# Performance work log

Measured on AMD Instinct MI355X. Metric: run time of the kernel, lower is better.

Reference implementation:

```python
import jax, jax.numpy as jnp
import numpy as np

EPS = 1e-8

def setup_inputs() -> dict:
    key = jax.random.key(0)
    k1, k2, k3, k4 = jax.random.split(key, 4)
    B, S, D = 64, 512, 512
    emb1 = jax.random.normal(k1, (B, S, D), dtype=jnp.float32)
    emb2 = jax.random.normal(k2, (B, S, D), dtype=jnp.float32)
    # contiguous prefix attention masks (first n tokens valid), as assumed by the original
    len1 = jax.random.randint(k3, (B,), S // 4, S + 1)
    len2 = jax.random.randint(k4, (B,), S // 4, S + 1)
    pos = jnp.arange(S)
    mask1 = (pos[None, :] < len1[:, None]).astype(jnp.int32)
    mask2 = (pos[None, :] < len2[:, None]).astype(jnp.int32)
    return {"article_1_emb": emb1, "article_2_emb": emb2,
            "article_1_att_mask": mask1, "article_2_att_mask": mask2}


def reference(article_1_emb, article_2_emb, article_1_att_mask, article_2_att_mask):
    # L2-normalize token embeddings (cosine similarity = dot of normalized vectors)
    def l2n(x):
        n = jnp.sqrt(jnp.sum(x * x, axis=-1, keepdims=True))
        return x / jnp.maximum(n, EPS)

    e1 = l2n(article_1_emb)   # [B, S1, D]
    e2 = l2n(article_2_emb)   # [B, S2, D]
    sim = jnp.einsum('bid,bjd->bij', e1, e2)  # [B, S1, S2] pairwise cosine sims

    m1 = article_1_att_mask.astype(jnp.bool_)  # [B, S1]
    m2 = article_2_att_mask.astype(jnp.bool_)  # [B, S2]
    NEG = jnp.float32(-1e9)

    # max over valid j for each valid i, and max over valid i for each valid j
    row_max = jnp.max(jnp.where(m2[:, None, :], sim, NEG), axis=2)  # [B, S1]
    col_max = jnp.max(jnp.where(m1[:, :, None], sim, NEG), axis=1)  # [B, S2]
    row_sum = jnp.sum(jnp.where(m1, row_max, 0.0), axis=1)          # [B]
    col_sum = jnp.sum(jnp.where(m2, col_max, 0.0), axis=1)          # [B]

    n1 = jnp.sum(article_1_att_mask, axis=1).astype(jnp.float32)
    n2 = jnp.sum(article_2_att_mask, axis=1).astype(jnp.float32)
    return (row_sum + col_sum) / (n1 + n2)
```

## Files before the change

### kernel.cpp

```cpp
#include <hip/hip_runtime.h>
#include <hip/hip_bf16.h>


typedef __attribute__((ext_vector_type(8))) short bf16x8;
typedef __attribute__((ext_vector_type(4))) float f32x4;

#define NEGBIG (-1e9f)
#define CAST_LDS(p) ((__attribute__((address_space(3))) void*)(p))
#define CAST_G(p)   ((const __attribute__((address_space(1))) void*)(p))

__device__ __forceinline__ unsigned bfbits(float f) {
    union { float f; unsigned u; } c; c.f = f;
    return (c.u + 0x7fffu + ((c.u >> 16) & 1u)) >> 16;
}
__device__ __forceinline__ unsigned packbf(float lo, float hi) {
    return (bfbits(hi) << 16) | bfbits(lo);
}

__global__ __launch_bounds__(256)
void prep_kernel(const float* __restrict__ e1, const float* __restrict__ e2,
                 ushort* __restrict__ n1, ushort* __restrict__ n2,
                 float* __restrict__ inv1, float* __restrict__ inv2)
{
    const int lane = threadIdx.x & 63;
    const int w    = threadIdx.x >> 6;
    const int row  = blockIdx.x * 4 + w;
    const bool is1 = row < 32768;
    const int  r   = is1 ? row : row - 32768;
    const float* src = (is1 ? e1 : e2) + (size_t)r * 512;
    ushort*      dst = (is1 ? n1 : n2) + (size_t)r * 512;

    const float4* s4 = reinterpret_cast<const float4*>(src);
    float4 a = s4[lane * 2];
    float4 c = s4[lane * 2 + 1];

    uint4 p;
    p.x = packbf(a.x, a.y);
    p.y = packbf(a.z, a.w);
    p.z = packbf(c.x, c.y);
    p.w = packbf(c.z, c.w);
    reinterpret_cast<uint4*>(dst)[lane] = p;

    float ss = a.x*a.x + a.y*a.y + a.z*a.z + a.w*a.w
             + c.x*c.x + c.y*c.y + c.z*c.z + c.w*c.w;
    #pragma unroll
    for (int m = 32; m; m >>= 1) ss += __shfl_xor(ss, m);
    if (lane == 0) {
        float iv = 1.0f / fmaxf(sqrtf(ss), 1e-8f);
        (is1 ? inv1 : inv2)[r] = iv;
    }
}

__global__ __launch_bounds__(256, 2)
void sim_kernel(const ushort* __restrict__ n1, const ushort* __restrict__ n2,
                const int* __restrict__ m1g, const int* __restrict__ m2g,
                const float* __restrict__ inv1, const float* __restrict__ inv2,
                float* __restrict__ rowmax_p,
                float* __restrict__ colmax_p)
{
    const int rt  = blockIdx.x;
    const int ct  = blockIdx.y;
    const int b   = blockIdx.z;
    const int tid = threadIdx.x;
    const int lane = tid & 63;
    const int w    = tid >> 6;
    const int wm   = w >> 1;
    const int wn   = w & 1;
    const int q    = lane >> 4;
    const int ln   = lane & 15;

    __shared__ __align__(16) ushort sA[128 * 32];
    __shared__ __align__(16) ushort sB[128 * 32];
    __shared__ float spr[2][128];
    __shared__ float spc[2][128];
    __shared__ int   sm1[128];
    __shared__ int   sm2[512];
    __shared__ float sinv1[128];
    __shared__ float sinv2[512];

    if (tid < 128) {
        sm1[tid]   = m1g[b * 512 + rt * 128 + tid];
        sinv1[tid] = inv1[b * 512 + rt * 128 + tid];
    }
    sm2[tid]         = m2g[b * 512 + tid];
    sm2[tid + 256]   = m2g[b * 512 + tid + 256];
    sinv2[tid]       = inv2[b * 512 + tid];
    sinv2[tid + 256] = inv2[b * 512 + tid + 256];

    const int gc = (lane & 3) ^ ((lane >> 2) & 3) ^ ((lane >> 4) & 3);
    const int r0 = w * 16 + (lane >> 2);
    const ushort* gA0 = n1 + (size_t)(b * 512 + rt * 128 + r0) * 512 + gc * 8;
    const ushort* gA1 = gA0 + 64 * 512;
    ushort* lA0 = sA + w * 512;
    ushort* lA1 = sA + 2048 + w * 512;
    ushort* lB0 = sB + w * 512;
    ushort* lB1 = sB + 2048 + w * 512;

    const int sln = (ln & 3) ^ ((ln >> 2) & 3);
    const ushort* aptr[4];
    const ushort* bptr[4];
    #pragma unroll
    for (int mt = 0; mt < 4; ++mt)
        aptr[mt] = &sA[(wm * 64 + mt * 16 + ln) * 32 + ((q ^ sln) << 3)];
    #pragma unroll
    for (int nt = 0; nt < 4; ++nt)
        bptr[nt] = &sB[(wn * 64 + nt * 16 + ln) * 32 + ((q ^ sln) << 3)];

    float runrow = NEGBIG;

    for (int nc = 0; nc < 2; ++nc) {
        const int nb = ct * 256 + nc * 128;
        const ushort* gB0 = n2 + (size_t)(b * 512 + nb + r0) * 512 + gc * 8;
        const ushort* gB1 = gB0 + 64 * 512;

        f32x4 acc[4][4];
        #pragma unroll
        for (int i = 0; i < 4; ++i)
            #pragma unroll
            for (int j = 0; j < 4; ++j)
                acc[i][j] = (f32x4){0.f, 0.f, 0.f, 0.f};

        for (int k0 = 0; k0 < 512; k0 += 32) {
            __syncthreads();
            __builtin_amdgcn_global_load_lds(CAST_G(gA0 + k0), CAST_LDS(lA0), 16, 0, 0);
            __builtin_amdgcn_global_load_lds(CAST_G(gA1 + k0), CAST_LDS(lA1), 16, 0, 0);
            __builtin_amdgcn_global_load_lds(CAST_G(gB0 + k0), CAST_LDS(lB0), 16, 0, 0);
            __builtin_amdgcn_global_load_lds(CAST_G(gB1 + k0), CAST_LDS(lB1), 16, 0, 0);
            __syncthreads();

            bf16x8 af[4], bfr[4];
            #pragma unroll
            for (int mt = 0; mt < 4; ++mt)
                af[mt] = *reinterpret_cast<const bf16x8*>(aptr[mt]);
            #pragma unroll
            for (int nt = 0; nt < 4; ++nt)
                bfr[nt] = *reinterpret_cast<const bf16x8*>(bptr[nt]);
            #pragma unroll
            for (int mt = 0; mt < 4; ++mt)
                #pragma unroll
                for (int nt = 0; nt < 4; ++nt)
                    acc[mt][nt] = __builtin_amdgcn_mfma_f32_16x16x32_bf16(
                        af[mt], bfr[nt], acc[mt][nt], 0, 0, 0);
        }

        float invj[4];
        f32x4 invi[4];
        #pragma unroll
        for (int nt = 0; nt < 4; ++nt)
            invj[nt] = sinv2[nb + wn * 64 + nt * 16 + ln];
        #pragma unroll
        for (int mt = 0; mt < 4; ++mt)
            #pragma unroll
            for (int rg = 0; rg < 4; ++rg)
                invi[mt][rg] = sinv1[wm * 64 + mt * 16 + q * 4 + rg];
        #pragma unroll
        for (int mt = 0; mt < 4; ++mt)
            #pragma unroll
            for (int nt = 0; nt < 4; ++nt)
                acc[mt][nt] = acc[mt][nt] * (invi[mt] * invj[nt]);

        #pragma unroll
        for (int mt = 0; mt < 4; ++mt) {
            #pragma unroll
            for (int rg = 0; rg < 4; ++rg) {
                float rm = NEGBIG;
                #pragma unroll
                for (int nt = 0; nt < 4; ++nt) {
                    int j = nb + wn * 64 + nt * 16 + ln;
                    float s = sm2[j] ? acc[mt][nt][rg] : NEGBIG;
                    rm = fmaxf(rm, s);
                }
                rm = fmaxf(rm, __shfl_xor(rm, 1));
                rm = fmaxf(rm, __shfl_xor(rm, 2));
                rm = fmaxf(rm, __shfl_xor(rm, 4));
                rm = fmaxf(rm, __shfl_xor(rm, 8));
                if (ln == 0) spr[wn][wm * 64 + mt * 16 + q * 4 + rg] = rm;
            }
        }
        #pragma unroll
        for (int nt = 0; nt < 4; ++nt) {
            float cm = NEGBIG;
            #pragma unroll
            for (int mt = 0; mt < 4; ++mt)
                #pragma unroll
                for (int rg = 0; rg < 4; ++rg) {
                    int il = wm * 64 + mt * 16 + q * 4 + rg;
                    float s = sm1[il] ? acc[mt][nt][rg] : NEGBIG;
                    cm = fmaxf(cm, s);
                }
            cm = fmaxf(cm, __shfl_xor(cm, 16));
            cm = fmaxf(cm, __shfl_xor(cm, 32));
            if (lane < 16) spc[wm][wn * 64 + nt * 16 + ln] = cm;
        }
        __syncthreads();
        if (tid < 128) {
            runrow = fmaxf(runrow, fmaxf(spr[0][tid], spr[1][tid]));
            colmax_p[((size_t)b * 4 + rt) * 512 + nb + tid] =
                fmaxf(spc[0][tid], spc[1][tid]);
        }
        __syncthreads();
    }
    if (tid < 128)
        rowmax_p[((size_t)b * 2 + ct) * 512 + rt * 128 + tid] = runrow;
}

__global__ __launch_bounds__(256)
void final_kernel(const int* __restrict__ m1g, const int* __restrict__ m2g,
                  const float* __restrict__ rowmax_p, const float* __restrict__ colmax_p,
                  float* __restrict__ out)
{
    const int b = blockIdx.x;
    const int tid = threadIdx.x;
    const int lane = tid & 63;
    const int w = tid >> 6;

    float sum = 0.f;
    float nn  = 0.f;
    for (int j = tid; j < 512; j += 256) {
        int mm1 = m1g[b * 512 + j];
        int mm2 = m2g[b * 512 + j];
        nn += (float)(mm1 + mm2);
        float rm = fmaxf(rowmax_p[(size_t)b * 1024 + j],
                         rowmax_p[(size_t)b * 1024 + 512 + j]);
        if (mm1) sum += rm;
        const float* cp = colmax_p + (size_t)b * 2048 + j;
        float cm = fmaxf(fmaxf(cp[0], cp[512]), fmaxf(cp[1024], cp[1536]));
        if (mm2) sum += cm;
    }
    #pragma unroll
    for (int m = 32; m; m >>= 1) {
        sum += __shfl_xor(sum, m);
        nn  += __shfl_xor(nn, m);
    }
    __shared__ float ssum[4], snn[4];
    if (lane == 0) { ssum[w] = sum; snn[w] = nn; }
    __syncthreads();
    if (tid == 0) {
        float S = ssum[0] + ssum[1] + ssum[2] + ssum[3];
        float N = snn[0] + snn[1] + snn[2] + snn[3];
        out[b] = S / N;
    }
}

__global__ __launch_bounds__(256)
void norm_kernel(const float* __restrict__ e1, const float* __restrict__ e2,
                 float* __restrict__ inv1, float* __restrict__ inv2)
{
    const int lane = threadIdx.x & 63;
    const int w    = threadIdx.x >> 6;
    const int row  = blockIdx.x * 4 + w;
    const float* src = (row < 32768) ? (e1 + (size_t)row * 512)
                                     : (e2 + (size_t)(row - 32768) * 512);
    const float4* s4 = reinterpret_cast<const float4*>(src);
    float4 a = s4[lane];
    float4 c = s4[lane + 64];
    float ss = a.x*a.x + a.y*a.y + a.z*a.z + a.w*a.w
             + c.x*c.x + c.y*c.y + c.z*c.z + c.w*c.w;
    #pragma unroll
    for (int m = 32; m; m >>= 1) ss += __shfl_xor(ss, m);
    if (lane == 0) {
        float iv = 1.0f / fmaxf(sqrtf(ss), 1e-8f);
        if (row < 32768) inv1[row] = iv; else inv2[row - 32768] = iv;
    }
}

__global__ __launch_bounds__(256, 2)
void sim_kernel_f32(const float* __restrict__ e1, const float* __restrict__ e2,
                    const int* __restrict__ m1g, const int* __restrict__ m2g,
                    const float* __restrict__ inv1, const float* __restrict__ inv2,
                    float* __restrict__ rowmax_p, float* __restrict__ colmax_p)
{
    const int rt  = blockIdx.x;
    const int ct  = blockIdx.y;
    const int b   = blockIdx.z;
    const int tid = threadIdx.x;
    const int lane = tid & 63;
    const int w    = tid >> 6;
    const int wm   = w >> 1;
    const int wn   = w & 1;
    const int q    = lane >> 4;
    const int ln   = lane & 15;

    __shared__ __align__(16) short sA[128 * 40];
    __shared__ __align__(16) short sB[128 * 40];
    __shared__ float spr[2][128];
    __shared__ float spc[2][128];
    __shared__ int   sm1[128];
    __shared__ int   sm2[512];

    if (tid < 128) sm1[tid] = m1g[b * 512 + rt * 128 + tid];
    sm2[tid]       = m2g[b * 512 + tid];
    sm2[tid + 256] = m2g[b * 512 + tid + 256];

    const int rA = tid >> 1;
    const int h  = tid & 1;
    const size_t baseA = ((size_t)(b * 512 + rt * 128 + rA)) * 512 + h * 16;
    const float iA = inv1[b * 512 + rt * 128 + rA];

    float runrow = NEGBIG;

    for (int nc = 0; nc < 2; ++nc) {
        const int nb = ct * 256 + nc * 128;
        const size_t baseB = ((size_t)(b * 512 + nb + rA)) * 512 + h * 16;
        const float iB = inv2[b * 512 + nb + rA];

        f32x4 acc[4][4];
        #pragma unroll
        for (int i = 0; i < 4; ++i)
            #pragma unroll
            for (int j = 0; j < 4; ++j)
                acc[i][j] = (f32x4){0.f, 0.f, 0.f, 0.f};

        for (int k0 = 0; k0 < 512; k0 += 32) {
            __syncthreads();
            {
                const float4* s4 = reinterpret_cast<const float4*>(e1 + baseA + k0);
                float4 v0 = s4[0], v1 = s4[1], v2 = s4[2], v3 = s4[3];
                uint4 p;
                p.x = packbf(v0.x * iA, v0.y * iA);
                p.y = packbf(v0.z * iA, v0.w * iA);
                p.z = packbf(v1.x * iA, v1.y * iA);
                p.w = packbf(v1.z * iA, v1.w * iA);
                *reinterpret_cast<uint4*>(&sA[rA * 40 + h * 16]) = p;
                p.x = packbf(v2.x * iA, v2.y * iA);
                p.y = packbf(v2.z * iA, v2.w * iA);
                p.z = packbf(v3.x * iA, v3.y * iA);
                p.w = packbf(v3.z * iA, v3.w * iA);
                *reinterpret_cast<uint4*>(&sA[rA * 40 + h * 16 + 8]) = p;
            }
            {
                const float4* s4 = reinterpret_cast<const float4*>(e2 + baseB + k0);
                float4 v0 = s4[0], v1 = s4[1], v2 = s4[2], v3 = s4[3];
                uint4 p;
                p.x = packbf(v0.x * iB, v0.y * iB);
                p.y = packbf(v0.z * iB, v0.w * iB);
                p.z = packbf(v1.x * iB, v1.y * iB);
                p.w = packbf(v1.z * iB, v1.w * iB);
                *reinterpret_cast<uint4*>(&sB[rA * 40 + h * 16]) = p;
                p.x = packbf(v2.x * iB, v2.y * iB);
                p.y = packbf(v2.z * iB, v2.w * iB);
                p.z = packbf(v3.x * iB, v3.y * iB);
                p.w = packbf(v3.z * iB, v3.w * iB);
                *reinterpret_cast<uint4*>(&sB[rA * 40 + h * 16 + 8]) = p;
            }
            __syncthreads();
            bf16x8 af[4], bfr[4];
            #pragma unroll
            for (int mt = 0; mt < 4; ++mt)
                af[mt] = *reinterpret_cast<const bf16x8*>(&sA[(wm * 64 + mt * 16 + ln) * 40 + q * 8]);
            #pragma unroll
            for (int nt = 0; nt < 4; ++nt)
                bfr[nt] = *reinterpret_cast<const bf16x8*>(&sB[(wn * 64 + nt * 16 + ln) * 40 + q * 8]);
            #pragma unroll
            for (int mt = 0; mt < 4; ++mt)
                #pragma unroll
                for (int nt = 0; nt < 4; ++nt)
                    acc[mt][nt] = __builtin_amdgcn_mfma_f32_16x16x32_bf16(
                        af[mt], bfr[nt], acc[mt][nt], 0, 0, 0);
        }

        #pragma unroll
        for (int mt = 0; mt < 4; ++mt) {
            #pragma unroll
            for (int rg = 0; rg < 4; ++rg) {
                float rm = NEGBIG;
                #pragma unroll
                for (int nt = 0; nt < 4; ++nt) {
                    int j = nb + wn * 64 + nt * 16 + ln;
                    float s = sm2[j] ? acc[mt][nt][rg] : NEGBIG;
                    rm = fmaxf(rm, s);
                }
                rm = fmaxf(rm, __shfl_xor(rm, 1));
                rm = fmaxf(rm, __shfl_xor(rm, 2));
                rm = fmaxf(rm, __shfl_xor(rm, 4));
                rm = fmaxf(rm, __shfl_xor(rm, 8));
                if (ln == 0) spr[wn][wm * 64 + mt * 16 + q * 4 + rg] = rm;
            }
        }
        #pragma unroll
        for (int nt = 0; nt < 4; ++nt) {
            float cm = NEGBIG;
            #pragma unroll
            for (int mt = 0; mt < 4; ++mt)
                #pragma unroll
                for (int rg = 0; rg < 4; ++rg) {
                    int il = wm * 64 + mt * 16 + q * 4 + rg;
                    float s = sm1[il] ? acc[mt][nt][rg] : NEGBIG;
                    cm = fmaxf(cm, s);
                }
            cm = fmaxf(cm, __shfl_xor(cm, 16));
            cm = fmaxf(cm, __shfl_xor(cm, 32));
            if (lane < 16) spc[wm][wn * 64 + nt * 16 + ln] = cm;
        }
        __syncthreads();
        if (tid < 128) {
            runrow = fmaxf(runrow, fmaxf(spr[0][tid], spr[1][tid]));
            colmax_p[((size_t)b * 4 + rt) * 512 + nb + tid] =
                fmaxf(spc[0][tid], spc[1][tid]);
        }
        __syncthreads();
    }
    if (tid < 128)
        rowmax_p[((size_t)b * 2 + ct) * 512 + rt * 128 + tid] = runrow;
}

extern "C" void kernel_launch(void* const* d_in, const int* in_sizes, int n_in,
                              void* d_out, int out_size, void* d_ws, size_t ws_size,
                              hipStream_t stream) {
    const float* e1 = (const float*)d_in[0];
    const float* e2 = (const float*)d_in[1];
    const int*   m1 = (const int*)d_in[2];
    const int*   m2 = (const int*)d_in[3];
    float* out = (float*)d_out;

    const size_t NELEM = (size_t)64 * 512 * 512;
    const size_t need  = 2 * NELEM * sizeof(ushort)
                       + (32768 + 32768 + 65536 + 131072) * sizeof(float);

    if (ws_size >= need) {
        ushort* n1 = (ushort*)d_ws;
        ushort* n2 = n1 + NELEM;
        float* tail     = (float*)(n2 + NELEM);
        float* inv1     = tail;
        float* inv2     = tail + 32768;
        float* rowmax_p = tail + 65536;
        float* colmax_p = tail + 131072;
        prep_kernel<<<16384, 256, 0, stream>>>(e1, e2, n1, n2, inv1, inv2);
        sim_kernel<<<dim3(4, 2, 64), 256, 0, stream>>>(n1, n2, m1, m2, inv1, inv2,
                                                       rowmax_p, colmax_p);
        final_kernel<<<64, 256, 0, stream>>>(m1, m2, rowmax_p, colmax_p, out);
    } else {
        float* ws = (float*)d_ws;
        float* inv1     = ws;
        float* inv2     = ws + 32768;
        float* rowmax_p = ws + 65536;
        float* colmax_p = ws + 131072;
        norm_kernel<<<16384, 256, 0, stream>>>(e1, e2, inv1, inv2);
        sim_kernel_f32<<<dim3(4, 2, 64), 256, 0, stream>>>(e1, e2, m1, m2, inv1, inv2,
                                                           rowmax_p, colmax_p);
        final_kernel<<<64, 256, 0, stream>>>(m1, m2, rowmax_p, colmax_p, out);
    }
}
```

Measured before the change: 195.7 us.

## Double-buffer LDS in sim kernel, split column tiles, process two rows per prep wave

```diff
diff --git a/kernel.cpp b/kernel.cpp
--- a/kernel.cpp
+++ b/kernel.cpp
@@ -16,42 +16,62 @@
 __device__ __forceinline__ unsigned packbf(float lo, float hi) {
     return (bfbits(hi) << 16) | bfbits(lo);
 }
-
-__global__ __launch_bounds__(256)
+__device__ __forceinline__ unsigned packbf2_hw(float lo, float hi) {
+    __hip_bfloat162 h = __float22bfloat162_rn(float2{lo, hi});
+    union { __hip_bfloat162 h; unsigned u; } c; c.h = h;
+    return c.u;
+}
+
+__global__ __launch_bounds__(256, 4)
 void prep_kernel(const float* __restrict__ e1, const float* __restrict__ e2,
                  ushort* __restrict__ n1, ushort* __restrict__ n2,
                  float* __restrict__ inv1, float* __restrict__ inv2)
 {
     const int lane = threadIdx.x & 63;
     const int w    = threadIdx.x >> 6;
-    const int row  = blockIdx.x * 4 + w;
-    const bool is1 = row < 32768;
-    const int  r   = is1 ? row : row - 32768;
+    const int gw   = blockIdx.x * 4 + w;
+    const int row0 = gw * 2;
+    const bool is1 = row0 < 32768;
+    const int  r   = is1 ? row0 : row0 - 32768;
     const float* src = (is1 ? e1 : e2) + (size_t)r * 512;
     ushort*      dst = (is1 ? n1 : n2) + (size_t)r * 512;
-
-    const float4* s4 = reinterpret_cast<const float4*>(src);
-    float4 a = s4[lane * 2];
-    float4 c = s4[lane * 2 + 1];
-
-    uint4 p;
-    p.x = packbf(a.x, a.y);
-    p.y = packbf(a.z, a.w);
-    p.z = packbf(c.x, c.y);
-    p.w = packbf(c.z, c.w);
-    reinterpret_cast<uint4*>(dst)[lane] = p;
-
-    float ss = a.x*a.x + a.y*a.y + a.z*a.z + a.w*a.w
-             + c.x*c.x + c.y*c.y + c.z*c.z + c.w*c.w;
-    #pragma unroll
-    for (int m = 32; m; m >>= 1) ss += __shfl_xor(ss, m);
+    float*      invp = (is1 ? inv1 : inv2) + r;
+
+    float4 v[2][2];
+    #pragma unroll
+    for (int rr = 0; rr < 2; ++rr) {
+        const float4* s4 = reinterpret_cast<const float4*>(src + rr * 512);
+        v[rr][0] = s4[lane * 2];
+        v[rr][1] = s4[lane * 2 + 1];
+    }
+    #pragma unroll
+    for (int rr = 0; rr < 2; ++rr) {
+        uint4 p;
+        p.x = packbf2_hw(v[rr][0].x, v[rr][0].y);
+        p.y = packbf2_hw(v[rr][0].z, v[rr][0].w);
+        p.z = packbf2_hw(v[rr][1].x, v[rr][1].y);
+        p.w = packbf2_hw(v[rr][1].z, v[rr][1].w);
+        reinterpret_cast<uint4*>(dst + rr * 512)[lane] = p;
+    }
+    float ss[2];
+    #pragma unroll
+    for (int rr = 0; rr < 2; ++rr) {
+        float4 a = v[rr][0], c = v[rr][1];
+        ss[rr] = a.x*a.x + a.y*a.y + a.z*a.z + a.w*a.w
+               + c.x*c.x + c.y*c.y + c.z*c.z + c.w*c.w;
+    }
+    #pragma unroll
+    for (int m = 32; m; m >>= 1) {
+        ss[0] += __shfl_xor(ss[0], m);
+        ss[1] += __shfl_xor(ss[1], m);
+    }
     if (lane == 0) {
-        float iv = 1.0f / fmaxf(sqrtf(ss), 1e-8f);
-        (is1 ? inv1 : inv2)[r] = iv;
-    }
-}
-
-__global__ __launch_bounds__(256, 2)
+        invp[0] = 1.0f / fmaxf(sqrtf(ss[0]), 1e-8f);
+        invp[1] = 1.0f / fmaxf(sqrtf(ss[1]), 1e-8f);
+    }
+}
+
+__global__ __launch_bounds__(256, 4)
 void sim_kernel(const ushort* __restrict__ n1, const ushort* __restrict__ n2,
                 const int* __restrict__ m1g, const int* __restrict__ m2g,
                 const float* __restrict__ inv1, const float* __restrict__ inv2,
@@ -68,140 +88,133 @@
     const int wn   = w & 1;
     const int q    = lane >> 4;
     const int ln   = lane & 15;
-
-    __shared__ __align__(16) ushort sA[128 * 32];
-    __shared__ __align__(16) ushort sB[128 * 32];
+    const int nb   = ct * 128;
+
+    __shared__ __align__(16) ushort sA[2][128 * 32];
+    __shared__ __align__(16) ushort sB[2][128 * 32];
     __shared__ float spr[2][128];
     __shared__ float spc[2][128];
-    __shared__ int   sm1[128];
-    __shared__ int   sm2[512];
-    __shared__ float sinv1[128];
-    __shared__ float sinv2[512];
+    __shared__ int   sm1[128], sm2[128];
+    __shared__ float sinv1[128], sinv2[128];
 
     if (tid < 128) {
         sm1[tid]   = m1g[b * 512 + rt * 128 + tid];
         sinv1[tid] = inv1[b * 512 + rt * 128 + tid];
-    }
-    sm2[tid]         = m2g[b * 512 + tid];
-    sm2[tid + 256]   = m2g[b * 512 + tid + 256];
-    sinv2[tid]       = inv2[b * 512 + tid];
-    sinv2[tid + 256] = inv2[b * 512 + tid + 256];
+    } else {
+        int t = tid - 128;
+        sm2[t]   = m2g[b * 512 + nb + t];
+        sinv2[t] = inv2[b * 512 + nb + t];
+    }
 
     const int gc = (lane & 3) ^ ((lane >> 2) & 3) ^ ((lane >> 4) & 3);
     const int r0 = w * 16 + (lane >> 2);
     const ushort* gA0 = n1 + (size_t)(b * 512 + rt * 128 + r0) * 512 + gc * 8;
     const ushort* gA1 = gA0 + 64 * 512;
-    ushort* lA0 = sA + w * 512;
-    ushort* lA1 = sA + 2048 + w * 512;
-    ushort* lB0 = sB + w * 512;
-    ushort* lB1 = sB + 2048 + w * 512;
+    const ushort* gB0 = n2 + (size_t)(b * 512 + nb + r0) * 512 + gc * 8;
+    const ushort* gB1 = gB0 + 64 * 512;
 
     const int sln = (ln & 3) ^ ((ln >> 2) & 3);
-    const ushort* aptr[4];
-    const ushort* bptr[4];
+    int aoff[4], boff[4];
     #pragma unroll
     for (int mt = 0; mt < 4; ++mt)
-        aptr[mt] = &sA[(wm * 64 + mt * 16 + ln) * 32 + ((q ^ sln) << 3)];
+        aoff[mt] = (wm * 64 + mt * 16 + ln) * 32 + ((q ^ sln) << 3);
     #pragma unroll
     for (int nt = 0; nt < 4; ++nt)
-        bptr[nt] = &sB[(wn * 64 + nt * 16 + ln) * 32 + ((q ^ sln) << 3)];
-
-    float runrow = NEGBIG;
-
-    for (int nc = 0; nc < 2; ++nc) {
-        const int nb = ct * 256 + nc * 128;
-        const ushort* gB0 = n2 + (size_t)(b * 512 + nb + r0) * 512 + gc * 8;
-        const ushort* gB1 = gB0 + 64 * 512;
-
-        f32x4 acc[4][4];
-        #pragma unroll
-        for (int i = 0; i < 4; ++i)
-            #pragma unroll
-            for (int j = 0; j < 4; ++j)
-                acc[i][j] = (f32x4){0.f, 0.f, 0.f, 0.f};
-
-        for (int k0 = 0; k0 < 512; k0 += 32) {
-            __syncthreads();
-            __builtin_amdgcn_global_load_lds(CAST_G(gA0 + k0), CAST_LDS(lA0), 16, 0, 0);
-            __builtin_amdgcn_global_load_lds(CAST_G(gA1 + k0), CAST_LDS(lA1), 16, 0, 0);
-            __builtin_amdgcn_global_load_lds(CAST_G(gB0 + k0), CAST_LDS(lB0), 16, 0, 0);
-            __builtin_amdgcn_global_load_lds(CAST_G(gB1 + k0), CAST_LDS(lB1), 16, 0, 0);
-            __syncthreads();
-
-            bf16x8 af[4], bfr[4];
-            #pragma unroll
-            for (int mt = 0; mt < 4; ++mt)
-                af[mt] = *reinterpret_cast<const bf16x8*>(aptr[mt]);
+        boff[nt] = (wn * 64 + nt * 16 + ln) * 32 + ((q ^ sln) << 3);
+
+    f32x4 acc[4][4];
+    #pragma unroll
+    for (int i = 0; i < 4; ++i)
+        #pragma unroll
+        for (int j = 0; j < 4; ++j)
+            acc[i][j] = (f32x4){0.f, 0.f, 0.f, 0.f};
+
+    __builtin_amdgcn_global_load_lds(CAST_G(gA0), CAST_LDS(&sA[0][w * 512]), 16, 0, 0);
+    __builtin_amdgcn_global_load_lds(CAST_G(gA1), CAST_LDS(&sA[0][2048 + w * 512]), 16, 0, 0);
+    __builtin_amdgcn_global_load_lds(CAST_G(gB0), CAST_LDS(&sB[0][w * 512]), 16, 0, 0);
+    __builtin_amdgcn_global_load_lds(CAST_G(gB1), CAST_LDS(&sB[0][2048 + w * 512]), 16, 0, 0);
+    __syncthreads();
+
+    #pragma unroll 2
+    for (int k = 0; k < 16; ++k) {
+        const int p = k & 1;
+        if (k < 15) {
+            const int k1 = (k + 1) * 32;
+            __builtin_amdgcn_global_load_lds(CAST_G(gA0 + k1), CAST_LDS(&sA[p ^ 1][w * 512]), 16, 0, 0);
+            __builtin_amdgcn_global_load_lds(CAST_G(gA1 + k1), CAST_LDS(&sA[p ^ 1][2048 + w * 512]), 16, 0, 0);
+            __builtin_amdgcn_global_load_lds(CAST_G(gB0 + k1), CAST_LDS(&sB[p ^ 1][w * 512]), 16, 0, 0);
+            __builtin_amdgcn_global_load_lds(CAST_G(gB1 + k1), CAST_LDS(&sB[p ^ 1][2048 + w * 512]), 16, 0, 0);
+        }
+        bf16x8 af[4], bfr[4];
+        #pragma unroll
+        for (int mt = 0; mt < 4; ++mt)
+            af[mt] = *reinterpret_cast<const bf16x8*>(&sA[p][aoff[mt]]);
+        #pragma unroll
+        for (int nt = 0; nt < 4; ++nt)
+            bfr[nt] = *reinterpret_cast<const bf16x8*>(&sB[p][boff[nt]]);
+        #pragma unroll
+        for (int mt = 0; mt < 4; ++mt)
             #pragma unroll
             for (int nt = 0; nt < 4; ++nt)
-                bfr[nt] = *reinterpret_cast<const bf16x8*>(bptr[nt]);
-            #pragma unroll
-            for (int mt = 0; mt < 4; ++mt)
-                #pragma unroll
-                for (int nt = 0; nt < 4; ++nt)
-                    acc[mt][nt] = __builtin_amdgcn_mfma_f32_16x16x32_bf16(
-                        af[mt], bfr[nt], acc[mt][nt], 0, 0, 0);
-        }
-
-        float invj[4];
-        f32x4 invi[4];
+                acc[mt][nt] = __builtin_amdgcn_mfma_f32_16x16x32_bf16(
+                    af[mt], bfr[nt], acc[mt][nt], 0, 0, 0);
+        __syncthreads();
+    }
+
+    float invj[4];
+    f32x4 invi[4];
+    #pragma unroll
+    for (int nt = 0; nt < 4; ++nt)
+        invj[nt] = sinv2[wn * 64 + nt * 16 + ln];
+    #pragma unroll
+    for (int mt = 0; mt < 4; ++mt)
+        #pragma unroll
+        for (int rg = 0; rg < 4; ++rg)
+            invi[mt][rg] = sinv1[wm * 64 + mt * 16 + q * 4 + rg];
+    #pragma unroll
+    for (int mt = 0; mt < 4; ++mt)
         #pragma unroll
         for (int nt = 0; nt < 4; ++nt)
-            invj[nt] = sinv2[nb + wn * 64 + nt * 16 + ln];
+            acc[mt][nt] = acc[mt][nt] * (invi[mt] * invj[nt]);
+
+    #pragma unroll
+    for (int mt = 0; mt < 4; ++mt) {
+        #pragma unroll
+        for (int rg = 0; rg < 4; ++rg) {
+            float rm = NEGBIG;
+            #pragma unroll
+            for (int nt = 0; nt < 4; ++nt) {
+                float s = sm2[wn * 64 + nt * 16 + ln] ? acc[mt][nt][rg] : NEGBIG;
+                rm = fmaxf(rm, s);
+            }
+            rm = fmaxf(rm, __shfl_xor(rm, 1));
+            rm = fmaxf(rm, __shfl_xor(rm, 2));
+            rm = fmaxf(rm, __shfl_xor(rm, 4));
+            rm = fmaxf(rm, __shfl_xor(rm, 8));
+            if (ln == 0) spr[wn][wm * 64 + mt * 16 + q * 4 + rg] = rm;
+        }
+    }
+    #pragma unroll
+    for (int nt = 0; nt < 4; ++nt) {
+        float cm = NEGBIG;
         #pragma unroll
         for (int mt = 0; mt < 4; ++mt)
             #pragma unroll
-            for (int rg = 0; rg < 4; ++rg)
-                invi[mt][rg] = sinv1[wm * 64 + mt * 16 + q * 4 + rg];
-        #pragma unroll
-        for (int mt = 0; mt < 4; ++mt)
-            #pragma unroll
-            for (int nt = 0; nt < 4; ++nt)
-                acc[mt][nt] = acc[mt][nt] * (invi[mt] * invj[nt]);
-
-        #pragma unroll
-        for (int mt = 0; mt < 4; ++mt) {
-            #pragma unroll
             for (int rg = 0; rg < 4; ++rg) {
-                float rm = NEGBIG;
-                #pragma unroll
-                for (int nt = 0; nt < 4; ++nt) {
-                    int j = nb + wn * 64 + nt * 16 + ln;
-                    float s = sm2[j] ? acc[mt][nt][rg] : NEGBIG;
-                    rm = fmaxf(rm, s);
-                }
-                rm = fmaxf(rm, __shfl_xor(rm, 1));
-                rm = fmaxf(rm, __shfl_xor(rm, 2));
-                rm = fmaxf(rm, __shfl_xor(rm, 4));
-                rm = fmaxf(rm, __shfl_xor(rm, 8));
-                if (ln == 0) spr[wn][wm * 64 + mt * 16 + q * 4 + rg] = rm;
+                float s = sm1[wm * 64 + mt * 16 + q * 4 + rg] ? acc[mt][nt][rg] : NEGBIG;
+                cm = fmaxf(cm, s);
             }
-        }
-        #pragma unroll
-        for (int nt = 0; nt < 4; ++nt) {
-            float cm = NEGBIG;
-            #pragma unroll
-            for (int mt = 0; mt < 4; ++mt)
-                #pragma unroll
-                for (int rg = 0; rg < 4; ++rg) {
-                    int il = wm * 64 + mt * 16 + q * 4 + rg;
-                    float s = sm1[il] ? acc[mt][nt][rg] : NEGBIG;
-                    cm = fmaxf(cm, s);
-                }
-            cm = fmaxf(cm, __shfl_xor(cm, 16));
-            cm = fmaxf(cm, __shfl_xor(cm, 32));
-            if (lane < 16) spc[wm][wn * 64 + nt * 16 + ln] = cm;
-        }
-        __syncthreads();
-        if (tid < 128) {
-            runrow = fmaxf(runrow, fmaxf(spr[0][tid], spr[1][tid]));
-            colmax_p[((size_t)b * 4 + rt) * 512 + nb + tid] =
-                fmaxf(spc[0][tid], spc[1][tid]);
-        }
-        __syncthreads();
-    }
-    if (tid < 128)
-        rowmax_p[((size_t)b * 2 + ct) * 512 + rt * 128 + tid] = runrow;
+        cm = fmaxf(cm, __shfl_xor(cm, 16));
+        cm = fmaxf(cm, __shfl_xor(cm, 32));
+        if (lane < 16) spc[wm][wn * 64 + nt * 16 + ln] = cm;
+    }
+    __syncthreads();
+    if (tid < 128) {
+        rowmax_p[((size_t)b * 4 + ct) * 512 + rt * 128 + tid] =
+            fmaxf(spr[0][tid], spr[1][tid]);
+        colmax_p[((size_t)b * 4 + rt) * 512 + nb + tid] =
+            fmaxf(spc[0][tid], spc[1][tid]);
+    }
 }
 
 __global__ __launch_bounds__(256)
@@ -220,8 +233,8 @@
         int mm1 = m1g[b * 512 + j];
         int mm2 = m2g[b * 512 + j];
         nn += (float)(mm1 + mm2);
-        float rm = fmaxf(rowmax_p[(size_t)b * 1024 + j],
-                         rowmax_p[(size_t)b * 1024 + 512 + j]);
+        const float* rp = rowmax_p + (size_t)b * 2048 + j;
+        float rm = fmaxf(fmaxf(rp[0], rp[512]), fmaxf(rp[1024], rp[1536]));
         if (mm1) sum += rm;
         const float* cp = colmax_p + (size_t)b * 2048 + j;
         float cm = fmaxf(fmaxf(cp[0], cp[512]), fmaxf(cp[1024], cp[1536]));
@@ -400,8 +413,11 @@
         }
         __syncthreads();
     }
-    if (tid < 128)
-        rowmax_p[((size_t)b * 2 + ct) * 512 + rt * 128 + tid] = runrow;
+    if (tid < 128) {
+        float v = runrow;
+        rowmax_p[((size_t)b * 4 + 2 * ct) * 512 + rt * 128 + tid] = v;
+        rowmax_p[((size_t)b * 4 + 2 * ct + 1) * 512 + rt * 128 + tid] = v;
+    }
 }
 
 extern "C" void kernel_launch(void* const* d_in, const int* in_sizes, int n_in,
@@ -415,7 +431,7 @@
 
     const size_t NELEM = (size_t)64 * 512 * 512;
     const size_t need  = 2 * NELEM * sizeof(ushort)
-                       + (32768 + 32768 + 65536 + 131072) * sizeof(float);
+                       + (32768 + 32768 + 131072 + 131072) * sizeof(float);
 
     if (ws_size >= need) {
         ushort* n1 = (ushort*)d_ws;
@@ -424,9 +440,9 @@
         float* inv1     = tail;
         float* inv2     = tail + 32768;
         float* rowmax_p = tail + 65536;
-        float* colmax_p = tail + 131072;
-        prep_kernel<<<16384, 256, 0, stream>>>(e1, e2, n1, n2, inv1, inv2);
-        sim_kernel<<<dim3(4, 2, 64), 256, 0, stream>>>(n1, n2, m1, m2, inv1, inv2,
+        float* colmax_p = tail + 196608;
+        prep_kernel<<<8192, 256, 0, stream>>>(e1, e2, n1, n2, inv1, inv2);
+        sim_kernel<<<dim3(4, 4, 64), 256, 0, stream>>>(n1, n2, m1, m2, inv1, inv2,
                                                        rowmax_p, colmax_p);
         final_kernel<<<64, 256, 0, stream>>>(m1, m2, rowmax_p, colmax_p, out);
     } else {
@@ -434,7 +450,7 @@
         float* inv1     = ws;
         float* inv2     = ws + 32768;
         float* rowmax_p = ws + 65536;
-        float* colmax_p = ws + 131072;
+        float* colmax_p = ws + 196608;
         norm_kernel<<<16384, 256, 0, stream>>>(e1, e2, inv1, inv2);
         sim_kernel_f32<<<dim3(4, 2, 64), 256, 0, stream>>>(e1, e2, m1, m2, inv1, inv2,
                                                            rowmax_p, colmax_p);
```

After: 195.9 us. No clear change (+0.1%).
